# Performance work log

Measured on AMD Instinct MI355X. Metric: run time of the kernel, lower is better.

Reference implementation:

```python
import jax, jax.numpy as jnp
import numpy as np

# Static config (matches init_kwargs / module defaults)
H = W = 24           # patch grid per image (hardcoded in module)
N = H * W            # 576 patch tokens
B = 64               # batch of anyres patches
D = 1024             # CLIP-ViT-L hidden size
K = 144              # num_tokens_to_keep
TOPN = 2             # top_n_per_region (TOKEN_CONFIGS[128])
DIST_THR = float(np.sqrt(280.0))
PCT = 0.55           # penalty_threshold_percentile (THRE)


def setup_inputs() -> dict:
    key = jax.random.key(0)
    k1, k2, k3 = jax.random.split(key, 3)
    return {
        "hidden_states_for_aggregation": jax.random.normal(k1, (B, N, D), jnp.float32),
        "hidden_states_for_sim": jax.random.normal(k2, (B, N, D), jnp.float32),
        "cls_attention_map": jax.random.uniform(k3, (B, N), jnp.float32),
    }


def _dist_penalty():
    # penalty(i,j) = max(0, 1 - dist2d(i,j)/thr); [N, N]
    ys, xs = jnp.meshgrid(jnp.arange(H), jnp.arange(W), indexing='ij')
    coords = jnp.stack([ys, xs], axis=-1).reshape(-1, 2).astype(jnp.float32)
    diff = coords[:, None, :] - coords[None, :, :]
    dist = jnp.sqrt(jnp.sum(diff * diff, axis=-1))
    return 1.0 - jnp.minimum(dist / DIST_THR, 1.0)


def reference(hidden_states_for_aggregation, hidden_states_for_sim, cls_attention_map):
    metric = cls_attention_map                      # [B, N]
    # --- per-region (2x2) local top-n selection ---
    m2d = metric.reshape(B, H, W)
    # unfold(1,2,2).unfold(2,2,2) -> [B, H/2, W/2, 2, 2], flat to [B, nr, 4]
    regions = m2d.reshape(B, H // 2, 2, W // 2, 2).transpose(0, 1, 3, 2, 4)
    nr_h, nr_w = H // 2, W // 2
    nr = nr_h * nr_w
    regions = regions.reshape(B, nr, 4)
    _, loc_idx = jax.lax.top_k(regions, TOPN)       # [B, nr, TOPN]
    ly, lx = loc_idx // 2, loc_idx % 2
    rid = jnp.arange(nr)[None, :, None]
    gy = (rid // nr_w) * 2 + ly
    gx = (rid % nr_w) * 2 + lx
    cand = (gy * W + gx).reshape(B, -1)             # [B, nr*TOPN]
    # --- global top-K among candidates ---
    cand_scores = jnp.take_along_axis(metric, cand, axis=1)
    _, top_c = jax.lax.top_k(cand_scores, K)
    benchmark_indices = jnp.sort(jnp.take_along_axis(cand, top_c, axis=1), axis=1)  # [B, K]
    # --- similarity with distance penalty ---
    norm = jnp.linalg.norm(hidden_states_for_sim, axis=-1, keepdims=True)
    pn = hidden_states_for_sim / jnp.maximum(norm, 1e-12)
    sim = jnp.einsum('bnd,bmd->bnm', pn, pn)        # [B, N, N]
    agg_w = jax.nn.relu(sim) * _dist_penalty()      # [B, N, N]
    bscores = jnp.take_along_axis(metric, benchmark_indices, axis=1)    # [B, K]
    thr = jnp.quantile(bscores, PCT, axis=1, keepdims=True)
    high = bscores >= thr                            # [B, K]
    one_hot = benchmark_indices[:, :, None] == jnp.arange(N)[None, None, :]  # [B, K, N]
    # rows of high-attn tokens zeroed except their own (self) column
    spm = jnp.where(high[:, :, None] & (~one_hot), 0.0, 1.0)
    bw = jnp.take_along_axis(agg_w, benchmark_indices[:, :, None], axis=1) * spm
    bwn = bw / (jnp.sum(bw, axis=-1, keepdims=True) + 1e-8)
    bwn = jnp.where(one_hot, 1.0, bwn)               # scatter self-weight = 1
    aggregated = jnp.einsum('bkn,bnd->bkd', bwn, hidden_states_for_aggregation)
    return aggregated, benchmark_indices
```

## Files before the change

kernel.cpp:

```cpp
#include <hip/hip_runtime.h>
#include <hip/hip_bf16.h>
#include <stdint.h>

#define B_  64
#define N_  576
#define D_  1024
#define K_  144
#define HW_ 24
#define DIST_THR_F 16.733200530681511f

using bf16x8 = __attribute__((ext_vector_type(8))) short;
using f32x4  = __attribute__((ext_vector_type(4))) float;

__device__ __forceinline__ unsigned short f2bf(float f) {
    unsigned u = __float_as_uint(f);
    u += 0x7fffu + ((u >> 16) & 1u);
    return (unsigned short)(u >> 16);
}

__global__ __launch_bounds__(256) void k_normcast(const float* __restrict__ x,
                                                  unsigned short* __restrict__ pn) {
    int row  = blockIdx.x * 4 + (threadIdx.x >> 6);
    int lane = threadIdx.x & 63;
    const float4* src = reinterpret_cast<const float4*>(x + (size_t)row * D_);
    float4 v[4];
    float ss = 0.f;
#pragma unroll
    for (int q = 0; q < 4; q++) {
        v[q] = src[lane + 64 * q];
        ss += v[q].x * v[q].x + v[q].y * v[q].y + v[q].z * v[q].z + v[q].w * v[q].w;
    }
#pragma unroll
    for (int m = 32; m >= 1; m >>= 1) ss += __shfl_xor(ss, m, 64);
    float inv = 1.0f / fmaxf(sqrtf(ss), 1e-12f);
    ushort4* dst = reinterpret_cast<ushort4*>(pn + (size_t)row * D_);
#pragma unroll
    for (int q = 0; q < 4; q++) {
        ushort4 o;
        o.x = f2bf(v[q].x * inv); o.y = f2bf(v[q].y * inv);
        o.z = f2bf(v[q].z * inv); o.w = f2bf(v[q].w * inv);
        dst[lane + 64 * q] = o;
    }
}

__global__ __launch_bounds__(256) void k_select(const float* __restrict__ metric,
                                                int* __restrict__ bench_idx,
                                                int* __restrict__ high,
                                                float* __restrict__ out_idx,
                                                float* __restrict__ rowsum) {
    __shared__ float sm[N_];
    __shared__ float sc[512];
    __shared__ int   si[512];
    __shared__ unsigned smask[18];
    __shared__ int   wpref[18];
    __shared__ float thr_s;
    int b = blockIdx.x, tid = threadIdx.x;
    for (int i = tid; i < N_; i += 256) sm[i] = metric[b * N_ + i];
    if (tid < 18) smask[tid] = 0u;
    if (tid < 144) rowsum[b * K_ + tid] = 0.f;
    __syncthreads();
    if (tid < 144) {
        int ry = tid / 12, rx = tid - ry * 12;
        int base = ry * 48 + rx * 2;
        float vv[4] = { sm[base], sm[base + 1], sm[base + 24], sm[base + 25] };
        int   tk[4] = { base, base + 1, base + 24, base + 25 };
        int a0 = 0;
#pragma unroll
        for (int j = 1; j < 4; j++) if (vv[j] > vv[a0]) a0 = j;
        int a1 = -1;
#pragma unroll
        for (int j = 0; j < 4; j++) {
            if (j == a0) continue;
            if (a1 < 0 || vv[j] > vv[a1]) a1 = j;
        }
        sc[2 * tid]     = vv[a0]; si[2 * tid]     = tk[a0];
        sc[2 * tid + 1] = vv[a1]; si[2 * tid + 1] = tk[a1];
    }
    for (int i = 288 + tid; i < 512; i += 256) { sc[i] = -1e30f; si[i] = 0x7fffffff; }
    __syncthreads();
    for (int k = 2; k <= 512; k <<= 1) {
        for (int j = k >> 1; j > 0; j >>= 1) {
#pragma unroll 2
            for (int t = tid; t < 512; t += 256) {
                int ixj = t ^ j;
                if (ixj > t) {
                    float s1 = sc[t], s2 = sc[ixj];
                    int   i1 = si[t], i2 = si[ixj];
                    bool before = (s1 > s2) || (s1 == s2 && i1 < i2);
                    bool up = ((t & k) == 0);
                    if (up ? !before : before) {
                        sc[t] = s2; sc[ixj] = s1; si[t] = i2; si[ixj] = i1;
                    }
                }
            }
            __syncthreads();
        }
    }
    if (tid == 0) {
        float qpos = 0.55f * 143.0f;
        float g = qpos - 78.0f;
        thr_s = sc[65] * (1.0f - g) + sc[64] * g;
    }
    if (tid < 144) atomicOr(&smask[si[tid] >> 5], 1u << (si[tid] & 31));
    __syncthreads();
    if (tid == 0) {
        int acc = 0;
        for (int w = 0; w < 18; w++) { wpref[w] = acc; acc += __popc(smask[w]); }
    }
    __syncthreads();
    if (tid < 144) {
        int tok = si[tid], w = tok >> 5;
        int rank = wpref[w] + __popc(smask[w] & ((1u << (tok & 31)) - 1u));
        bench_idx[b * K_ + rank] = tok;
        high[b * K_ + rank] = (sc[tid] >= thr_s) ? 1 : 0;
        out_idx[b * K_ + rank] = (float)tok;
    }
}

__global__ __launch_bounds__(384) void k_sim9(const unsigned short* __restrict__ pn,
                                              const int* __restrict__ bench_idx,
                                              const int* __restrict__ high,
                                              unsigned short* __restrict__ bwn,
                                              float* __restrict__ rowsum) {
    __shared__ unsigned short SM[240 * 64];
    __shared__ float rsum[144];
    int bid  = blockIdx.x;
    int xcd  = bid & 7;
    int s    = bid >> 3;
    int ct   = s % 6;
    int b    = (s / 6) * 8 + xcd;
    int tid  = threadIdx.x;
    int w = tid >> 6, lane = tid & 63, g = lane >> 4, r16 = lane & 15;
    int wr = w >> 1, wc = w & 1;

    if (tid < 144) rsum[tid] = 0.f;

    const unsigned short* pnb = pn + (size_t)b * N_ * D_;

    const unsigned short* gsrc[5];
    int dsoff[5];
#pragma unroll
    for (int q = 0; q < 5; q++) {
        int cid = tid + 384 * q;
        int row = cid >> 3;
        int p   = cid & 7;
        int l   = p ^ (row & 7);
        int tok = (row < 144) ? bench_idx[b * K_ + row] : (ct * 96 + (row - 144));
        gsrc[q]  = pnb + (size_t)tok * D_ + l * 8;
        dsoff[q] = row * 64 + p * 8;
    }

    bf16x8 sreg[5];
#pragma unroll
    for (int q = 0; q < 5; q++) sreg[q] = *(const bf16x8*)(gsrc[q]);

    f32x4 acc[3][3] = {};

    for (int t = 0; t < 16; ++t) {
#pragma unroll
        for (int q = 0; q < 5; q++) *(bf16x8*)&SM[dsoff[q]] = sreg[q];
        __syncthreads();
        if (t < 15) {
            int kb = (t + 1) * 64;
#pragma unroll
            for (int q = 0; q < 5; q++) sreg[q] = *(const bf16x8*)(gsrc[q] + kb);
        }
#pragma unroll
        for (int h = 0; h < 2; h++) {
            int ks = h * 4 + g;
            bf16x8 af[3], bf[3];
#pragma unroll
            for (int mi = 0; mi < 3; mi++) {
                int row = wr * 48 + mi * 16 + r16;
                af[mi] = *(const bf16x8*)&SM[row * 64 + (ks ^ (row & 7)) * 8];
            }
#pragma unroll
            for (int nj = 0; nj < 3; nj++) {
                int row = 144 + wc * 48 + nj * 16 + r16;
                bf[nj] = *(const bf16x8*)&SM[row * 64 + (ks ^ (row & 7)) * 8];
            }
#pragma unroll
            for (int mi = 0; mi < 3; mi++)
#pragma unroll
                for (int nj = 0; nj < 3; nj++)
                    acc[mi][nj] = __builtin_amdgcn_mfma_f32_16x16x32_bf16(af[mi], bf[nj], acc[mi][nj], 0, 0, 0);
        }
        __syncthreads();
    }

#pragma unroll
    for (int mi = 0; mi < 3; mi++) {
#pragma unroll
        for (int r = 0; r < 4; r++) {
            int i = wr * 48 + mi * 16 + g * 4 + r;
            int ti = bench_idx[b * K_ + i];
            int hi = high[b * K_ + i];
            int y1 = ti / HW_, x1 = ti % HW_;
            unsigned short* prow = bwn + (size_t)(b * K_ + i) * N_;
            float vals[3];
            float sum3 = 0.f;
#pragma unroll
            for (int nj = 0; nj < 3; nj++) {
                int col = ct * 96 + wc * 48 + nj * 16 + r16;
                int y2 = col / HW_, x2 = col % HW_;
                float dy = (float)(y1 - y2), dx = (float)(x1 - x2);
                float dist = sqrtf(dy * dy + dx * dx);
                float pen = 1.0f - fminf(dist / DIST_THR_F, 1.0f);
                float v = fmaxf(acc[mi][nj][r], 0.0f) * pen;
                vals[nj] = v;
                sum3 += v;
            }
#pragma unroll
            for (int m = 1; m <= 8; m <<= 1) sum3 += __shfl_xor(sum3, m, 64);
            if (r16 == 0) atomicAdd(&rsum[i], sum3);
#pragma unroll
            for (int nj = 0; nj < 3; nj++) {
                int col = ct * 96 + wc * 48 + nj * 16 + r16;
                unsigned short o = (hi || col == ti) ? (unsigned short)0 : f2bf(vals[nj]);
                prow[col] = o;
            }
        }
    }
    __syncthreads();
    if (tid < 144) atomicAdd(&rowsum[b * K_ + tid], rsum[tid]);
}

__global__ __launch_bounds__(384) void k_agg5(const unsigned short* __restrict__ bwn,
                                              const float* __restrict__ agg,
                                              const int* __restrict__ bench_idx,
                                              const float* __restrict__ rowsum,
                                              float* __restrict__ out) {
    __shared__ unsigned short LA[144 * 64];
    __shared__ unsigned int   LB[256 * 32];
    int bid  = blockIdx.x;
    int xcd  = bid & 7;
    int s    = bid >> 3;
    int dt   = s & 3;
    int b    = (s >> 2) * 8 + xcd;
    int tid  = threadIdx.x;
    int w = tid >> 6, lane = tid & 63, g = lane >> 4, r16 = lane & 15;
    int wr = w >> 1, wc = w & 1;

    const unsigned short* asrc[3];
    int adso[3];
#pragma unroll
    for (int q = 0; q < 3; q++) {
        int cid = tid + 384 * q;
        int row = cid >> 3, p = cid & 7, l = p ^ (row & 7);
        asrc[q] = bwn + (size_t)(b * K_ + row) * N_ + l * 8;
        adso[q] = row * 64 + p * 8;
    }
    const float* bbase = agg + (size_t)b * N_ * D_ + dt * 256 + lane * 4;

    bf16x8 areg[3];
    float4 breg[6][2];
#pragma unroll
    for (int q = 0; q < 3; q++) areg[q] = *(const bf16x8*)(asrc[q]);
#pragma unroll
    for (int u = 0; u < 6; u++) {
        int pp = w + 6 * u;
        if (pp < 32) {
            breg[u][0] = *(const float4*)(bbase + (size_t)(2 * pp) * D_);
            breg[u][1] = *(const float4*)(bbase + (size_t)(2 * pp + 1) * D_);
        }
    }

    f32x4 acc[3][8] = {};

    for (int t = 0; t < 9; ++t) {
#pragma unroll
        for (int q = 0; q < 3; q++) *(bf16x8*)&LA[adso[q]] = areg[q];
#pragma unroll
        for (int u = 0; u < 6; u++) {
            int pp = w + 6 * u;
            if (pp < 32) {
                float a0[4] = { breg[u][0].x, breg[u][0].y, breg[u][0].z, breg[u][0].w };
                float a1[4] = { breg[u][1].x, breg[u][1].y, breg[u][1].z, breg[u][1].w };
                int js = pp >> 2;
#pragma unroll
                for (int c = 0; c < 4; c++) {
                    int d = lane * 4 + c;
                    int sw = (js ^ (d & 7) ^ ((d >> 3) & 7)) & 7;
                    unsigned pk = (unsigned)f2bf(a0[c]) | ((unsigned)f2bf(a1[c]) << 16);
                    LB[d * 32 + sw * 4 + (pp & 3)] = pk;
                }
            }
        }
        __syncthreads();
        if (t < 8) {
            int kb = (t + 1) * 64;
#pragma unroll
            for (int q = 0; q < 3; q++) areg[q] = *(const bf16x8*)(asrc[q] + kb);
#pragma unroll
            for (int u = 0; u < 6; u++) {
                int pp = w + 6 * u;
                if (pp < 32) {
                    breg[u][0] = *(const float4*)(bbase + (size_t)(kb + 2 * pp) * D_);
                    breg[u][1] = *(const float4*)(bbase + (size_t)(kb + 2 * pp + 1) * D_);
                }
            }
        }
#pragma unroll
        for (int h = 0; h < 2; h++) {
            int ks = h * 4 + g;
            bf16x8 af[3], bf[8];
#pragma unroll
            for (int mi = 0; mi < 3; mi++) {
                int row = wr * 48 + mi * 16 + r16;
                af[mi] = *(const bf16x8*)&LA[row * 64 + (ks ^ (row & 7)) * 8];
            }
#pragma unroll
            for (int nj = 0; nj < 8; nj++) {
                int d = wc * 128 + nj * 16 + r16;
                int sw = (ks ^ (d & 7) ^ ((d >> 3) & 7)) & 7;
                bf[nj] = *(const bf16x8*)&LB[d * 32 + sw * 4];
            }
#pragma unroll
            for (int mi = 0; mi < 3; mi++)
#pragma unroll
                for (int nj = 0; nj < 8; nj++)
                    acc[mi][nj] = __builtin_amdgcn_mfma_f32_16x16x32_bf16(af[mi], bf[nj], acc[mi][nj], 0, 0, 0);
        }
        __syncthreads();
    }

#pragma unroll
    for (int mi = 0; mi < 3; mi++) {
#pragma unroll
        for (int r = 0; r < 4; r++) {
            int i = wr * 48 + mi * 16 + g * 4 + r;
            float S = rowsum[b * K_ + i];
            float sc = 1.0f / (S + 1e-8f);
            int ti = bench_idx[b * K_ + i];
            const float* selfrow = agg + (size_t)(b * N_ + ti) * D_ + dt * 256 + wc * 128;
            float* orow = out + (size_t)(b * K_ + i) * D_ + dt * 256 + wc * 128;
#pragma unroll
            for (int nj = 0; nj < 8; nj++)
                orow[nj * 16 + r16] = acc[mi][nj][r] * sc + selfrow[nj * 16 + r16];
        }
    }
}

extern "C" void kernel_launch(void* const* d_in, const int* in_sizes, int n_in,
                              void* d_out, int out_size, void* d_ws, size_t ws_size,
                              hipStream_t stream) {
    const float* hs_agg = (const float*)d_in[0];
    const float* hs_sim = (const float*)d_in[1];
    const float* metric = (const float*)d_in[2];
    float* out = (float*)d_out;
    char* ws = (char*)d_ws;

    const size_t PN_BYTES  = (size_t)B_ * N_ * D_ * 2;
    const size_t BWN_BYTES = (size_t)B_ * K_ * N_ * 2;
    unsigned short* pn  = (unsigned short*)ws;
    unsigned short* bwn = (unsigned short*)(ws + PN_BYTES);
    int*   bench_idx = (int*)(ws + PN_BYTES + BWN_BYTES);
    int*   high      = (int*)(ws + PN_BYTES + BWN_BYTES + (size_t)B_ * K_ * 4);
    float* rowsum    = (float*)(ws + PN_BYTES + BWN_BYTES + (size_t)B_ * K_ * 8);
    float* out_idx   = out + (size_t)B_ * K_ * D_;

    hipLaunchKernelGGL(k_normcast, dim3((B_ * N_) / 4), dim3(256), 0, stream, hs_sim, pn);
    hipLaunchKernelGGL(k_select,   dim3(B_),            dim3(256), 0, stream, metric, bench_idx, high, out_idx, rowsum);
    hipLaunchKernelGGL(k_sim9,     dim3(B_ * 6),        dim3(384), 0, stream, pn, bench_idx, high, bwn, rowsum);
    hipLaunchKernelGGL(k_agg5,     dim3(B_ * 4),        dim3(384), 0, stream, bwn, hs_agg, bench_idx, rowsum, out);
}
```

Measured before the change: 131.9 us.

## Fuse normalize and select kernels; split similarity GEMM into smaller row tiles

Combines the normalize-cast and token-selection kernels into one launch, with block index ranges dispatching to each role. Retiles the similarity GEMM from 144x96 output tiles with 6 waves to 48x96 tiles with 2 waves, giving three times more blocks and smaller shared memory per block. The aim is better occupancy and CU coverage plus one fewer launch. The cost is reloading each column panel three times, which adds global and L2 traffic.

Result: faster. 128.1 us (-2.9%).

```diff
diff --git a/kernel.cpp b/kernel.cpp
--- a/kernel.cpp
+++ b/kernel.cpp
@@ -18,43 +18,44 @@
     return (unsigned short)(u >> 16);
 }
 
-__global__ __launch_bounds__(256) void k_normcast(const float* __restrict__ x,
-                                                  unsigned short* __restrict__ pn) {
-    int row  = blockIdx.x * 4 + (threadIdx.x >> 6);
-    int lane = threadIdx.x & 63;
-    const float4* src = reinterpret_cast<const float4*>(x + (size_t)row * D_);
-    float4 v[4];
-    float ss = 0.f;
-#pragma unroll
-    for (int q = 0; q < 4; q++) {
-        v[q] = src[lane + 64 * q];
-        ss += v[q].x * v[q].x + v[q].y * v[q].y + v[q].z * v[q].z + v[q].w * v[q].w;
-    }
-#pragma unroll
-    for (int m = 32; m >= 1; m >>= 1) ss += __shfl_xor(ss, m, 64);
-    float inv = 1.0f / fmaxf(sqrtf(ss), 1e-12f);
-    ushort4* dst = reinterpret_cast<ushort4*>(pn + (size_t)row * D_);
-#pragma unroll
-    for (int q = 0; q < 4; q++) {
-        ushort4 o;
-        o.x = f2bf(v[q].x * inv); o.y = f2bf(v[q].y * inv);
-        o.z = f2bf(v[q].z * inv); o.w = f2bf(v[q].w * inv);
-        dst[lane + 64 * q] = o;
-    }
-}
-
-__global__ __launch_bounds__(256) void k_select(const float* __restrict__ metric,
-                                                int* __restrict__ bench_idx,
-                                                int* __restrict__ high,
-                                                float* __restrict__ out_idx,
-                                                float* __restrict__ rowsum) {
+__global__ __launch_bounds__(256) void k_prep(const float* __restrict__ x,
+                                              unsigned short* __restrict__ pn,
+                                              const float* __restrict__ metric,
+                                              int* __restrict__ bench_idx,
+                                              int* __restrict__ high,
+                                              float* __restrict__ out_idx,
+                                              float* __restrict__ rowsum) {
+    if (blockIdx.x < 9216) {
+        int row  = blockIdx.x * 4 + (threadIdx.x >> 6);
+        int lane = threadIdx.x & 63;
+        const float4* src = reinterpret_cast<const float4*>(x + (size_t)row * D_);
+        float4 v[4];
+        float ss = 0.f;
+#pragma unroll
+        for (int q = 0; q < 4; q++) {
+            v[q] = src[lane + 64 * q];
+            ss += v[q].x * v[q].x + v[q].y * v[q].y + v[q].z * v[q].z + v[q].w * v[q].w;
+        }
+#pragma unroll
+        for (int m = 32; m >= 1; m >>= 1) ss += __shfl_xor(ss, m, 64);
+        float inv = 1.0f / fmaxf(sqrtf(ss), 1e-12f);
+        ushort4* dst = reinterpret_cast<ushort4*>(pn + (size_t)row * D_);
+#pragma unroll
+        for (int q = 0; q < 4; q++) {
+            ushort4 o;
+            o.x = f2bf(v[q].x * inv); o.y = f2bf(v[q].y * inv);
+            o.z = f2bf(v[q].z * inv); o.w = f2bf(v[q].w * inv);
+            dst[lane + 64 * q] = o;
+        }
+        return;
+    }
     __shared__ float sm[N_];
     __shared__ float sc[512];
     __shared__ int   si[512];
     __shared__ unsigned smask[18];
     __shared__ int   wpref[18];
     __shared__ float thr_s;
-    int b = blockIdx.x, tid = threadIdx.x;
+    int b = blockIdx.x - 9216, tid = threadIdx.x;
     for (int i = tid; i < N_; i += 256) sm[i] = metric[b * N_ + i];
     if (tid < 18) smask[tid] = 0u;
     if (tid < 144) rowsum[b * K_ + tid] = 0.f;
@@ -117,53 +118,53 @@
     }
 }
 
-__global__ __launch_bounds__(384) void k_sim9(const unsigned short* __restrict__ pn,
-                                              const int* __restrict__ bench_idx,
-                                              const int* __restrict__ high,
-                                              unsigned short* __restrict__ bwn,
-                                              float* __restrict__ rowsum) {
-    __shared__ unsigned short SM[240 * 64];
-    __shared__ float rsum[144];
+__global__ __launch_bounds__(128) void k_sim11(const unsigned short* __restrict__ pn,
+                                               const int* __restrict__ bench_idx,
+                                               const int* __restrict__ high,
+                                               unsigned short* __restrict__ bwn,
+                                               float* __restrict__ rowsum) {
+    __shared__ unsigned short SM[144 * 64];
+    __shared__ float rsum[48];
     int bid  = blockIdx.x;
     int xcd  = bid & 7;
-    int s    = bid >> 3;
-    int ct   = s % 6;
-    int b    = (s / 6) * 8 + xcd;
+    int slot = bid >> 3;
+    int s18  = slot % 18;
+    int b    = (slot / 18) * 8 + xcd;
+    int rt   = s18 / 6;
+    int ct   = s18 % 6;
     int tid  = threadIdx.x;
     int w = tid >> 6, lane = tid & 63, g = lane >> 4, r16 = lane & 15;
-    int wr = w >> 1, wc = w & 1;
-
-    if (tid < 144) rsum[tid] = 0.f;
+
+    if (tid < 48) rsum[tid] = 0.f;
 
     const unsigned short* pnb = pn + (size_t)b * N_ * D_;
 
-    const unsigned short* gsrc[5];
-    int dsoff[5];
-#pragma unroll
-    for (int q = 0; q < 5; q++) {
-        int cid = tid + 384 * q;
-        int row = cid >> 3;
-        int p   = cid & 7;
+    const unsigned short* gsrc[9];
+    int dsoff[9];
+#pragma unroll
+    for (int q = 0; q < 9; q++) {
+        int row = (tid >> 3) + 16 * q;
+        int p   = tid & 7;
         int l   = p ^ (row & 7);
-        int tok = (row < 144) ? bench_idx[b * K_ + row] : (ct * 96 + (row - 144));
+        int tok = (row < 48) ? bench_idx[b * K_ + rt * 48 + row] : (ct * 96 + (row - 48));
         gsrc[q]  = pnb + (size_t)tok * D_ + l * 8;
         dsoff[q] = row * 64 + p * 8;
     }
 
-    bf16x8 sreg[5];
-#pragma unroll
-    for (int q = 0; q < 5; q++) sreg[q] = *(const bf16x8*)(gsrc[q]);
+    bf16x8 sreg[9];
+#pragma unroll
+    for (int q = 0; q < 9; q++) sreg[q] = *(const bf16x8*)(gsrc[q]);
 
     f32x4 acc[3][3] = {};
 
     for (int t = 0; t < 16; ++t) {
 #pragma unroll
-        for (int q = 0; q < 5; q++) *(bf16x8*)&SM[dsoff[q]] = sreg[q];
+        for (int q = 0; q < 9; q++) *(bf16x8*)&SM[dsoff[q]] = sreg[q];
         __syncthreads();
         if (t < 15) {
             int kb = (t + 1) * 64;
 #pragma unroll
-            for (int q = 0; q < 5; q++) sreg[q] = *(const bf16x8*)(gsrc[q] + kb);
+            for (int q = 0; q < 9; q++) sreg[q] = *(const bf16x8*)(gsrc[q] + kb);
         }
 #pragma unroll
         for (int h = 0; h < 2; h++) {
@@ -171,12 +172,12 @@
             bf16x8 af[3], bf[3];
 #pragma unroll
             for (int mi = 0; mi < 3; mi++) {
-                int row = wr * 48 + mi * 16 + r16;
+                int row = mi * 16 + r16;
                 af[mi] = *(const bf16x8*)&SM[row * 64 + (ks ^ (row & 7)) * 8];
             }
 #pragma unroll
             for (int nj = 0; nj < 3; nj++) {
-                int row = 144 + wc * 48 + nj * 16 + r16;
+                int row = 48 + w * 48 + nj * 16 + r16;
                 bf[nj] = *(const bf16x8*)&SM[row * 64 + (ks ^ (row & 7)) * 8];
             }
 #pragma unroll
@@ -192,7 +193,8 @@
     for (int mi = 0; mi < 3; mi++) {
 #pragma unroll
         for (int r = 0; r < 4; r++) {
-            int i = wr * 48 + mi * 16 + g * 4 + r;
+            int il = mi * 16 + g * 4 + r;
+            int i  = rt * 48 + il;
             int ti = bench_idx[b * K_ + i];
             int hi = high[b * K_ + i];
             int y1 = ti / HW_, x1 = ti % HW_;
@@ -201,7 +203,7 @@
             float sum3 = 0.f;
 #pragma unroll
             for (int nj = 0; nj < 3; nj++) {
-                int col = ct * 96 + wc * 48 + nj * 16 + r16;
+                int col = ct * 96 + w * 48 + nj * 16 + r16;
                 int y2 = col / HW_, x2 = col % HW_;
                 float dy = (float)(y1 - y2), dx = (float)(x1 - x2);
                 float dist = sqrtf(dy * dy + dx * dx);
@@ -212,17 +214,17 @@
             }
 #pragma unroll
             for (int m = 1; m <= 8; m <<= 1) sum3 += __shfl_xor(sum3, m, 64);
-            if (r16 == 0) atomicAdd(&rsum[i], sum3);
+            if (r16 == 0) atomicAdd(&rsum[il], sum3);
 #pragma unroll
             for (int nj = 0; nj < 3; nj++) {
-                int col = ct * 96 + wc * 48 + nj * 16 + r16;
+                int col = ct * 96 + w * 48 + nj * 16 + r16;
                 unsigned short o = (hi || col == ti) ? (unsigned short)0 : f2bf(vals[nj]);
                 prow[col] = o;
             }
         }
     }
     __syncthreads();
-    if (tid < 144) atomicAdd(&rowsum[b * K_ + tid], rsum[tid]);
+    if (tid < 48) atomicAdd(&rowsum[b * K_ + rt * 48 + tid], rsum[tid]);
 }
 
 __global__ __launch_bounds__(384) void k_agg5(const unsigned short* __restrict__ bwn,
@@ -359,8 +361,10 @@
     float* rowsum    = (float*)(ws + PN_BYTES + BWN_BYTES + (size_t)B_ * K_ * 8);
     float* out_idx   = out + (size_t)B_ * K_ * D_;
 
-    hipLaunchKernelGGL(k_normcast, dim3((B_ * N_) / 4), dim3(256), 0, stream, hs_sim, pn);
-    hipLaunchKernelGGL(k_select,   dim3(B_),            dim3(256), 0, stream, metric, bench_idx, high, out_idx, rowsum);
-    hipLaunchKernelGGL(k_sim9,     dim3(B_ * 6),        dim3(384), 0, stream, pn, bench_idx, high, bwn, rowsum);
-    hipLaunchKernelGGL(k_agg5,     dim3(B_ * 4),        dim3(384), 0, stream, bwn, hs_agg, bench_idx, rowsum, out);
-}
+    hipLaunchKernelGGL(k_prep,  dim3(9216 + B_), dim3(256), 0, stream,
+                       hs_sim, pn, metric, bench_idx, high, out_idx, rowsum);
+    hipLaunchKernelGGL(k_sim11, dim3(B_ * 18),   dim3(128), 0, stream,
+                       pn, bench_idx, high, bwn, rowsum);
+    hipLaunchKernelGGL(k_agg5,  dim3(B_ * 4),    dim3(384), 0, stream,
+                       bwn, hs_agg, bench_idx, rowsum, out);
+}
```
